# Kernel tuning notes

Measured on AMD Instinct MI355X. Metric: run time of the kernel, lower is better.

The kernel has to match this reference:

```python
import jax, jax.numpy as jnp
import numpy as np

N = 100000            # total buses
H = 64                # hidden_channels
OUT = 4               # out_channels
E = 100000            # edges per relation
EPF = 800000          # power-flow edges
# node-type global index ranges: SB, PV, PQ, NB
TYPE_RANGES = [(0, 10000), (10000, 30000), (30000, 70000), (70000, 100000)]
# 14 unique relations (src_type, dst_type) matching the HeteroConv dict order
RELS = [(0,1),(0,2),(0,3),(1,2),(1,3),(2,3),(1,0),(2,0),(3,0),(2,1),(3,2),(1,1),(2,2),(3,3)]
NUM_REL = len(RELS)


def custom_sigmoid(v, lo, hi, slope=0.1):
    mid = (lo + hi) * 0.5
    s = 1.0 / (1.0 + jnp.exp(-slope * (v - mid)))
    return (s - 0.5) * (hi - lo) + mid


def setup_inputs() -> dict:
    key = jax.random.key(0)
    ks = jax.random.split(key, 32)
    # node features (kept away from 0: x[:,0] is a divisor in the PF update)
    x = jax.random.uniform(ks[0], (N, 4)) + 0.5
    # constraints: [v_lo, v_hi, s_max, p_lo, p_hi, q_lo, q_hi] with lo < hi
    b = jax.random.uniform(ks[1], (N, 7))
    constraints = jnp.stack([b[:, 0], b[:, 0] + 1.0, b[:, 2],
                             b[:, 3] - 1.0, b[:, 3] + 1.0,
                             b[:, 5] - 1.0, b[:, 5] + 1.0], axis=1)
    rng = np.random.default_rng(0)
    edge_src = np.stack([rng.integers(TYPE_RANGES[s][0], TYPE_RANGES[s][1], size=E)
                         for s, _ in RELS]).astype(np.int32)
    edge_dst = np.stack([rng.integers(TYPE_RANGES[d][0], TYPE_RANGES[d][1], size=E)
                         for _, d in RELS]).astype(np.int32)
    edge_attr = jax.random.uniform(ks[2], (NUM_REL, E, 2)) + 0.5   # (R, X) > 0
    pf_i = jnp.asarray(rng.integers(0, N, size=EPF).astype(np.int32))
    pf_j = jnp.asarray(rng.integers(0, N, size=EPF).astype(np.int32))
    pf_attr = jax.random.uniform(ks[3], (EPF, 2)) + 0.5

    def W(k, *shape):
        return jax.random.normal(k, shape) * 0.05

    p = {}
    # layer 0 convs: in=4 ; layer 1 convs: in=H. Per-relation stacked weights.
    names = ['Wq', 'bq', 'Wk', 'bk', 'Wv', 'bv', 'We', 'Ws', 'bs']
    for layer, din in [(0, 4), (1, H)]:
        kk = jax.random.split(ks[4 + layer], 9)
        shapes = [(NUM_REL, din, H), (NUM_REL, H), (NUM_REL, din, H), (NUM_REL, H),
                  (NUM_REL, din, H), (NUM_REL, H), (NUM_REL, 2, H),
                  (NUM_REL, din, H), (NUM_REL, H)]
        for nm, sk, sh in zip(names, kk, shapes):
            p[f'{nm}{layer}'] = W(sk, *sh)
    Wlin = W(ks[6], H, OUT)
    return dict(x=x, constraints=constraints,
                edge_src=jnp.asarray(edge_src), edge_dst=jnp.asarray(edge_dst),
                edge_attr=edge_attr, pf_i=pf_i, pf_j=pf_j, pf_attr=pf_attr,
                Wlin=Wlin, **p)


def _hetero_layer(h, params, edge_src, edge_dst, edge_attr):
    """One HeteroConv(TransformerConv, aggr='sum') layer over global node array h[N,din]."""
    Wq, bq, Wk, bk, Wv, bv, We, Ws, bs = params
    n = h.shape[0]
    scale = Wq.shape[-1] ** -0.5
    out = jnp.zeros((n, Wq.shape[-1]), h.dtype)
    for r in range(NUM_REL):
        dlo, dhi = TYPE_RANGES[RELS[r][1]]
        s, d = edge_src[r], edge_dst[r]
        hs = h[s]                                    # [E, din] gathered src feats
        eemb = edge_attr[r] @ We[r]                  # lin_edge (no bias)
        kmat = hs @ Wk[r] + bk[r] + eemb             # key_j + edge
        vmat = hs @ Wv[r] + bv[r]                    # value_j
        q_dst = h[dlo:dhi] @ Wq[r] + bq[r]           # query on dst-type nodes only
        alpha = jnp.sum(q_dst[d - dlo] * kmat, axis=-1) * scale
        # segment softmax over incoming edges per dst node (per relation)
        m = jax.ops.segment_max(alpha, d, num_segments=n)
        a = jnp.exp(alpha - m[d])
        den = jax.ops.segment_sum(a, d, num_segments=n)
        a = a / (den[d] + 1e-16)
        out = out + jax.ops.segment_sum(a[:, None] * (vmat + eemb), d, num_segments=n)
        # root/skip connection (per relation, summed by HeteroConv aggr='sum')
        out = out.at[dlo:dhi].add(h[dlo:dhi] @ Ws[r] + bs[r])
    return out


def _forward(x, constraints, edge_attr, pf_attr, p0, p1, Wlin,
             edge_src, edge_dst, pf_i, pf_j):
    h = jax.nn.relu(_hetero_layer(x, p0, edge_src, edge_dst, edge_attr))
    h = jax.nn.relu(_hetero_layer(h, p1, edge_src, edge_dst, edge_attr))
    out = h @ Wlin                                   # [N, 4], lin (no bias)
    # vectorized per-bus power flow (edge-parallel gather-compute-scatter)
    V = jnp.abs(out[:, 0])
    th = out[:, 1]
    r_, x_ = pf_attr[:, 0], pf_attr[:, 1]
    den = r_ * r_ + x_ * x_
    G = r_ / den
    B = -x_ / den
    dlt = th[pf_j] - th[pf_i]
    cd, sd = jnp.cos(dlt), jnp.sin(dlt)
    vv = V[pf_i] * V[pf_j]
    P = jax.ops.segment_sum(vv * (G * cd + B * sd), pf_i, num_segments=N)
    Q = jax.ops.segment_sum(vv * (G * sd - B * cd), pf_i, num_segments=N)
    o0 = custom_sigmoid(V, constraints[:, 0], constraints[:, 1]) / x[:, 0]
    o2 = custom_sigmoid(P, constraints[:, 3], constraints[:, 4])
    o3 = custom_sigmoid(Q, constraints[:, 5], constraints[:, 6])
    return out.at[:, 0].set(o0).at[:, 2].set(o2).at[:, 3].set(o3)


def reference(x, constraints, edge_src, edge_dst, edge_attr, pf_i, pf_j, pf_attr,
              Wq0, bq0, Wk0, bk0, Wv0, bv0, We0, Ws0, bs0,
              Wq1, bq1, Wk1, bk1, Wv1, bv1, We1, Ws1, bs1, Wlin):
    p0 = (Wq0, bq0, Wk0, bk0, Wv0, bv0, We0, Ws0, bs0)
    p1 = (Wq1, bq1, Wk1, bk1, Wv1, bv1, We1, Ws1, bs1)
    return _forward(x, constraints, edge_attr, pf_attr, p0, p1, Wlin,
                    edge_src, edge_dst, pf_i, pf_j)
```

## Files before the change

### kernel.cpp

```cpp
#include <hip/hip_runtime.h>
#include <hip/hip_bf16.h>

#define NREL 14
#define NE     100000
#define NEDGE  (NREL*NE)
#define NN     100000
#define EPF    800000
#define NQ     370000
#define NB1    ((NQ + 1023) / 1024)
#define QWAVES 5786
#define TWAVES 1564

__device__ __constant__ int d_dlo[NREL]   = {10000,30000,70000,30000,70000,70000,0,0,0,10000,30000,10000,30000,70000};
__device__ __constant__ int d_qoff[NREL+1]= {0,20000,60000,90000,130000,160000,190000,200000,210000,220000,240000,280000,300000,340000,370000};
__device__ __constant__ int d_qwoff[NREL+1]={0,313,938,1407,2032,2501,2970,3127,3284,3441,3754,4379,4692,5317,5786};
__device__ __constant__ int d_trel[4][4]  = {{6,7,8,-1},{0,9,11,-1},{1,3,10,12},{2,4,5,13}};
__device__ __constant__ int d_ntrel[4]    = {3,3,4,4};
__device__ __constant__ int d_tbase[5]    = {0,10000,30000,70000,100000};
__device__ __constant__ int d_twoff[5]    = {0,157,470,1095,1564};

__device__ __forceinline__ float csig(float v, float lo, float hi) {
    float mid = 0.5f * (lo + hi);
    float s = 1.0f / (1.0f + expf(-0.1f * (v - mid)));
    return (s - 0.5f) * (hi - lo) + mid;
}

template<int K>
__device__ __forceinline__ void stage_in(
    float* sIn, const float* __restrict__ src, int l0, int n, int tid)
{
    if (K == 4) {
        if (tid < 64) {
            int lcl = min(l0 + tid, n - 1);
            float4 v = *(const float4*)(src + (long)lcl * 4);
            sIn[0 * 64 + tid] = v.x; sIn[1 * 64 + tid] = v.y;
            sIn[2 * 64 + tid] = v.z; sIn[3 * 64 + tid] = v.w;
        }
    } else {
        int row = tid >> 2, q = tid & 3;
        int lcl = min(l0 + row, n - 1);
        const float* p = src + (long)lcl * 64 + q * 16;
        #pragma unroll
        for (int kk = 0; kk < 4; ++kk) {
            float4 v = *(const float4*)(p + kk * 4);
            int k = q * 16 + kk * 4;
            sIn[(k + 0) * 64 + row] = v.x;
            sIn[(k + 1) * 64 + row] = v.y;
            sIn[(k + 2) * 64 + row] = v.z;
            sIn[(k + 3) * 64 + row] = v.w;
        }
    }
}

template<int K>
__device__ __forceinline__ void stage_w(
    float* sW, const float* __restrict__ src, int tid)
{
    for (int i = tid * 4; i < K * 64; i += 1024)
        *(float4*)(sW + i) = *(const float4*)(src + i);
}

template<int K>
__device__ __forceinline__ void mma_t(
    float acc[4][4], const float* sIn, const float* sW, int r0, int c0)
{
    for (int k = 0; k < K; ++k) {
        float4 a = *(const float4*)(sIn + k * 64 + r0);
        float4 b = *(const float4*)(sW + k * 64 + c0);
        acc[0][0] = fmaf(a.x, b.x, acc[0][0]);
        acc[0][1] = fmaf(a.x, b.y, acc[0][1]);
        acc[0][2] = fmaf(a.x, b.z, acc[0][2]);
        acc[0][3] = fmaf(a.x, b.w, acc[0][3]);
        acc[1][0] = fmaf(a.y, b.x, acc[1][0]);
        acc[1][1] = fmaf(a.y, b.y, acc[1][1]);
        acc[1][2] = fmaf(a.y, b.z, acc[1][2]);
        acc[1][3] = fmaf(a.y, b.w, acc[1][3]);
        acc[2][0] = fmaf(a.z, b.x, acc[2][0]);
        acc[2][1] = fmaf(a.z, b.y, acc[2][1]);
        acc[2][2] = fmaf(a.z, b.z, acc[2][2]);
        acc[2][3] = fmaf(a.z, b.w, acc[2][3]);
        acc[3][0] = fmaf(a.w, b.x, acc[3][0]);
        acc[3][1] = fmaf(a.w, b.y, acc[3][1]);
        acc[3][2] = fmaf(a.w, b.z, acc[3][2]);
        acc[3][3] = fmaf(a.w, b.w, acc[3][3]);
    }
}

template<int DIN>
__global__ __launch_bounds__(256) void combine_skip(
    const float* __restrict__ Ws, float* __restrict__ Wc)
{
    int tid = blockIdx.x * blockDim.x + threadIdx.x;
    if (tid >= 4 * DIN * 64) return;
    int t = tid / (DIN * 64), o = tid % (DIN * 64);
    float s = 0.f;
    for (int ri = 0; ri < d_ntrel[t]; ++ri) s += Ws[d_trel[t][ri] * DIN * 64 + o];
    Wc[tid] = s;
}

template<int DIN>
__global__ __launch_bounds__(256) void mk_m2t(
    const float* __restrict__ Wk, const float* __restrict__ Wq,
    float* __restrict__ M2T)
{
    int tid = blockIdx.x * blockDim.x + threadIdx.x;
    if (tid >= NREL * DIN * DIN) return;
    int r = tid / (DIN * DIN), rem = tid % (DIN * DIN);
    int i = rem / DIN, j = rem % DIN;
    const float* wki = Wk + (long)r * DIN * 64 + i * 64;
    const float* wqj = Wq + (long)r * DIN * 64 + j * 64;
    float s = 0.f;
    for (int c = 0; c < 64; ++c) s = fmaf(wki[c], wqj[c], s);
    M2T[(long)r * DIN * DIN + j * DIN + i] = s;
}

template<int DIN>
__global__ __launch_bounds__(256) void mk_vecs(
    const float* __restrict__ Wk, const float* __restrict__ Wq,
    const float* __restrict__ bq, const float* __restrict__ bk,
    const float* __restrict__ We, float* __restrict__ vec4)
{
    int tid = blockIdx.x * blockDim.x + threadIdx.x;
    if (tid >= NREL * 4 * DIN) return;
    int r = tid / (4 * DIN), rem = tid % (4 * DIN);
    int k = rem / DIN, i = rem % DIN;
    const float* row; const float* v;
    if (k == 0) { row = Wk + (long)r * DIN * 64 + i * 64; v = bq + r * 64; }
    else {
        row = Wq + (long)r * DIN * 64 + i * 64;
        v = (k == 1) ? We + r * 128 : (k == 2) ? We + r * 128 + 64 : bk + r * 64;
    }
    float s = 0.f;
    for (int c = 0; c < 64; ++c) s = fmaf(row[c], v[c], s);
    vec4[tid] = s;
}

__global__ __launch_bounds__(64) void mk_scl(
    const float* __restrict__ bq, const float* __restrict__ bk,
    const float* __restrict__ We, float* __restrict__ scl)
{
    int r = blockIdx.x * blockDim.x + threadIdx.x;
    if (r >= NREL) return;
    float s0 = 0.f, s1 = 0.f, sb = 0.f;
    for (int c = 0; c < 64; ++c) {
        float b = bq[r * 64 + c];
        s0 = fmaf(b, We[r * 128 + c], s0);
        s1 = fmaf(b, We[r * 128 + 64 + c], s1);
        sb = fmaf(b, bk[r * 64 + c], sb);
    }
    scl[4 * r] = s0; scl[4 * r + 1] = s1; scl[4 * r + 2] = sb; scl[4 * r + 3] = 0.f;
}

__global__ __launch_bounds__(256) void dstprep4(
    const float* __restrict__ h, const float* __restrict__ M2T,
    const float* __restrict__ vec4, const float* __restrict__ scl,
    float* __restrict__ ug, float* __restrict__ scal)
{
    int idx = blockIdx.x * blockDim.x + threadIdx.x;
    if (idx >= NQ) return;
    int r = 0;
    while (r < NREL - 1 && idx >= d_qoff[r + 1]) ++r;
    int node = d_dlo[r] + (idx - d_qoff[r]);
    float4 hv = ((const float4*)h)[node];
    const float* m2 = M2T + (long)r * 16;
    const float* vb = vec4 + (long)r * 16;
    float u[4];
    #pragma unroll
    for (int c = 0; c < 4; ++c)
        u[c] = vb[c] + hv.x * m2[c] + hv.y * m2[4 + c] + hv.z * m2[8 + c] + hv.w * m2[12 + c];
    float sc0 = scl[4*r]   + hv.x*vb[4]  + hv.y*vb[5]  + hv.z*vb[6]  + hv.w*vb[7];
    float sc1 = scl[4*r+1] + hv.x*vb[8]  + hv.y*vb[9]  + hv.z*vb[10] + hv.w*vb[11];
    float scb = scl[4*r+2] + hv.x*vb[12] + hv.y*vb[13] + hv.z*vb[14] + hv.w*vb[15];
    ((float4*)ug)[idx] = make_float4(u[0], u[1], u[2], u[3]);
    ((float4*)scal)[idx] = make_float4(sc0, sc1, scb, 0.f);
}

__global__ __launch_bounds__(256) void dstprep_g(
    const float* __restrict__ h, const float* __restrict__ M2T,
    const float* __restrict__ vec4, const float* __restrict__ scl,
    float* __restrict__ ug, float* __restrict__ scal)
{
    __shared__ float sIn[64 * 64];
    __shared__ float sW[64 * 64];
    int blk = blockIdx.x, tid = threadIdx.x;
    int r = 0;
    while (r < NREL - 1 && blk >= d_qwoff[r + 1]) ++r;
    int l0 = (blk - d_qwoff[r]) * 64;
    int nd = d_qoff[r + 1] - d_qoff[r];
    stage_in<64>(sIn, h + (long)d_dlo[r] * 64, l0, nd, tid);
    stage_w<64>(sW, M2T + (long)r * 4096, tid);
    __syncthreads();
    int tx = tid & 15, ty = tid >> 4;
    int r0 = ty * 4, c0 = tx * 4;
    float4 bias = *(const float4*)(vec4 + (long)r * 256 + c0);
    float acc[4][4];
    #pragma unroll
    for (int i = 0; i < 4; ++i) {
        acc[i][0] = bias.x; acc[i][1] = bias.y; acc[i][2] = bias.z; acc[i][3] = bias.w;
    }
    mma_t<64>(acc, sIn, sW, r0, c0);
    #pragma unroll
    for (int i = 0; i < 4; ++i) {
        int lr = l0 + r0 + i;
        if (lr < nd)
            *(float4*)(ug + (long)(d_qoff[r] + lr) * 64 + c0) =
                make_float4(acc[i][0], acc[i][1], acc[i][2], acc[i][3]);
    }
    if (tid < 64) {
        const float* w1p = vec4 + (long)r * 256 + 64;
        const float* w2p = vec4 + (long)r * 256 + 128;
        const float* w3p = vec4 + (long)r * 256 + 192;
        float s0 = 0.f, s1 = 0.f, s2 = 0.f;
        for (int k = 0; k < 64; ++k) {
            float hv = sIn[k * 64 + tid];
            s0 = fmaf(hv, w1p[k], s0);
            s1 = fmaf(hv, w2p[k], s1);
            s2 = fmaf(hv, w3p[k], s2);
        }
        int lr = l0 + tid;
        if (lr < nd)
            ((float4*)scal)[d_qoff[r] + lr] =
                make_float4(s0 + scl[4*r], s1 + scl[4*r+1], s2 + scl[4*r+2], 0.f);
    }
}

__global__ __launch_bounds__(256) void csr_count(
    const int* __restrict__ edst, int* __restrict__ cur)
{
    int tid = blockIdx.x * blockDim.x + threadIdx.x;
    if (tid >= NEDGE) return;
    int r = tid / NE;
    atomicAdd(&cur[d_qoff[r] + edst[tid] - d_dlo[r]], 1);
}

__global__ __launch_bounds__(1024) void scan1(
    const int* __restrict__ cur, int* __restrict__ rowst, int* __restrict__ bsum)
{
    __shared__ int s[1024];
    int t = threadIdx.x, g = blockIdx.x * 1024 + t;
    s[t] = g < NQ ? cur[g] : 0;
    __syncthreads();
    for (int o = 1; o < 1024; o <<= 1) {
        int x = t >= o ? s[t - o] : 0;
        __syncthreads();
        s[t] += x;
        __syncthreads();
    }
    if (g < NQ) rowst[g + 1] = s[t];
    if (t == 1023) bsum[blockIdx.x] = s[1023];
}

__global__ __launch_bounds__(512) void scan2(int* __restrict__ bsum)
{
    __shared__ int s[512];
    int t = threadIdx.x;
    s[t] = t < NB1 ? bsum[t] : 0;
    __syncthreads();
    for (int o = 1; o < 512; o <<= 1) {
        int x = t >= o ? s[t - o] : 0;
        __syncthreads();
        s[t] += x;
        __syncthreads();
    }
    if (t < NB1) bsum[t] = (t == 0) ? 0 : s[t - 1];
}

__global__ __launch_bounds__(256) void scan3(
    const int* __restrict__ bsum, int* __restrict__ rowst)
{
    int g = blockIdx.x * blockDim.x + threadIdx.x;
    if (g == 0) rowst[0] = 0;
    if (g < NQ) rowst[g + 1] += bsum[g >> 10];
}

__global__ __launch_bounds__(256) void csr_fill(
    const int* __restrict__ edst, const int* __restrict__ rowst,
    int* __restrict__ cur, int* __restrict__ elist)
{
    int tid = blockIdx.x * blockDim.x + threadIdx.x;
    if (tid >= NEDGE) return;
    int r = tid / NE;
    int idx = d_qoff[r] + edst[tid] - d_dlo[r];
    int pos = rowst[idx] + atomicAdd(&cur[idx], 1);
    elist[pos] = tid;
}

__global__ __launch_bounds__(256) void gfuse_t4(
    const float* __restrict__ h, const float* __restrict__ scal,
    const int* __restrict__ esrc, const float* __restrict__ eattr,
    const int* __restrict__ rowst, const int* __restrict__ elist,
    float* __restrict__ ug, float* __restrict__ gm)
{
    int idx = blockIdx.x * blockDim.x + threadIdx.x;
    if (idx >= NQ) return;
    int e0 = rowst[idx], e1 = rowst[idx + 1];
    if (e0 == e1) {
        ((float4*)ug)[idx] = make_float4(0.f, 0.f, 0.f, 0.f);
        gm[2 * (long)idx] = 0.f; gm[2 * (long)idx + 1] = 0.f;
        return;
    }
    float4 u = ((const float4*)ug)[idx];
    float4 sc = ((const float4*)scal)[idx];
    float m = -3.4e38f, den = 0.f, m0 = 0.f, m1 = 0.f;
    float gx = 0.f, gy = 0.f, gz = 0.f, gw = 0.f;
    for (int e = e0; e < e1; ++e) {
        int eid = elist[e];
        float4 hs = ((const float4*)h)[esrc[eid]];
        float2 ea = *(const float2*)(eattr + 2 * (long)eid);
        float alpha = 0.125f * (hs.x*u.x + hs.y*u.y + hs.z*u.z + hs.w*u.w
                                + sc.z + ea.x * sc.x + ea.y * sc.y);
        float nm = fmaxf(m, alpha);
        float s = expf(m - nm);
        float a = expf(alpha - nm);
        m = nm;
        den = den * s + a;
        gx = gx * s + a * hs.x; gy = gy * s + a * hs.y;
        gz = gz * s + a * hs.z; gw = gw * s + a * hs.w;
        m0 = m0 * s + a * ea.x; m1 = m1 * s + a * ea.y;
    }
    float inv = 1.f / (den + 1e-16f);
    ((float4*)ug)[idx] = make_float4(gx*inv, gy*inv, gz*inv, gw*inv);
    gm[2 * (long)idx] = m0 * inv; gm[2 * (long)idx + 1] = m1 * inv;
}

__global__ __launch_bounds__(256) void gfuse_q(
    const float* __restrict__ h, const float* __restrict__ scal,
    const int* __restrict__ esrc, const float* __restrict__ eattr,
    const int* __restrict__ rowst, const int* __restrict__ elist,
    float* __restrict__ ug, float* __restrict__ gm)
{
    int idx = (blockIdx.x * blockDim.x + threadIdx.x) >> 4;
    int ql  = threadIdx.x & 15;
    if (idx >= NQ) return;
    int e0 = rowst[idx], e1 = rowst[idx + 1];
    long ubase = (long)idx * 64 + ql * 4;
    if (e0 == e1) {
        *(float4*)(ug + ubase) = make_float4(0.f, 0.f, 0.f, 0.f);
        if (ql == 0) { gm[2*(long)idx] = 0.f; gm[2*(long)idx+1] = 0.f; }
        return;
    }
    float4 u = *(const float4*)(ug + ubase);
    float4 sc = ((const float4*)scal)[idx];
    float m = -3.4e38f, den = 0.f, m0 = 0.f, m1 = 0.f;
    float4 g = make_float4(0.f, 0.f, 0.f, 0.f);
    for (int e = e0; e < e1; ++e) {
        int eid = elist[e];
        int s = esrc[eid];
        float2 ea = *(const float2*)(eattr + 2 * (long)eid);
        float4 hs = *(const float4*)(h + (long)s * 64 + ql * 4);
        float p = hs.x*u.x + hs.y*u.y + hs.z*u.z + hs.w*u.w;
        p += __shfl_xor(p, 1);
        p += __shfl_xor(p, 2);
        p += __shfl_xor(p, 4);
        p += __shfl_xor(p, 8);
        float alpha = 0.125f * (p + sc.z + ea.x * sc.x + ea.y * sc.y);
        float nm = fmaxf(m, alpha);
        float s0 = expf(m - nm);
        float a  = expf(alpha - nm);
        m = nm;
        den = den * s0 + a;
        g.x = g.x * s0 + a * hs.x;
        g.y = g.y * s0 + a * hs.y;
        g.z = g.z * s0 + a * hs.z;
        g.w = g.w * s0 + a * hs.w;
        m0 = m0 * s0 + a * ea.x;
        m1 = m1 * s0 + a * ea.y;
    }
    float inv = 1.f / (den + 1e-16f);
    *(float4*)(ug + ubase) = make_float4(g.x*inv, g.y*inv, g.z*inv, g.w*inv);
    if (ql == 0) { gm[2*(long)idx] = m0 * inv; gm[2*(long)idx+1] = m1 * inv; }
}

template<int K, int RELU>
__global__ __launch_bounds__(256) void combine_g(
    const float* __restrict__ h, const float* __restrict__ Wc,
    const float* __restrict__ bs, const float* __restrict__ Wv,
    const float* __restrict__ bv, const float* __restrict__ We,
    const float* __restrict__ ug, const float* __restrict__ gm,
    const int* __restrict__ rowst, float* __restrict__ outp)
{
    __shared__ float sIn[K * 64];
    __shared__ float sW[K * 64];
    __shared__ float sHe[64], sG0[64], sG1[64];
    int blk = blockIdx.x, tid = threadIdx.x;
    int t = 0;
    while (t < 3 && blk >= d_twoff[t + 1]) ++t;
    int l0 = (blk - d_twoff[t]) * 64;
    int nt = d_tbase[t + 1] - d_tbase[t];
    int tx = tid & 15, ty = tid >> 4;
    int r0 = ty * 4, c0 = tx * 4;
    float acc[4][4];
    #pragma unroll
    for (int i = 0; i < 4; ++i) {
        acc[i][0] = 0.f; acc[i][1] = 0.f; acc[i][2] = 0.f; acc[i][3] = 0.f;
    }
    stage_in<K>(sIn, h + (long)d_tbase[t] * K, l0, nt, tid);
    stage_w<K>(sW, Wc + (long)t * K * 64, tid);
    __syncthreads();
    mma_t<K>(acc, sIn, sW, r0, c0);
    int nr = d_ntrel[t];
    for (int ri = 0; ri < nr; ++ri) {
        int rr = d_trel[t][ri];
        __syncthreads();
        stage_in<K>(sIn, ug + (long)d_qoff[rr] * K, l0, nt, tid);
        stage_w<K>(sW, Wv + (long)rr * K * 64, tid);
        if (tid < 64) {
            int lcl = min(l0 + tid, nt - 1);
            long idx = d_qoff[rr] + lcl;
            sHe[tid] = (rowst[idx + 1] > rowst[idx]) ? 1.f : 0.f;
            sG0[tid] = gm[2 * idx];
            sG1[tid] = gm[2 * idx + 1];
        }
        __syncthreads();
        mma_t<K>(acc, sIn, sW, r0, c0);
        float4 bsr = *(const float4*)(bs + rr * 64 + c0);
        float4 bvr = *(const float4*)(bv + rr * 64 + c0);
        float4 w0  = *(const float4*)(We + rr * 128 + c0);
        float4 w1  = *(const float4*)(We + rr * 128 + 64 + c0);
        #pragma unroll
        for (int i = 0; i < 4; ++i) {
            float he = sHe[r0 + i], g0 = sG0[r0 + i], g1 = sG1[r0 + i];
            acc[i][0] += bsr.x + he * bvr.x + g0 * w0.x + g1 * w1.x;
            acc[i][1] += bsr.y + he * bvr.y + g0 * w0.y + g1 * w1.y;
            acc[i][2] += bsr.z + he * bvr.z + g0 * w0.z + g1 * w1.z;
            acc[i][3] += bsr.w + he * bvr.w + g0 * w0.w + g1 * w1.w;
        }
    }
    #pragma unroll
    for (int i = 0; i < 4; ++i) {
        int lr = l0 + r0 + i;
        if (lr < nt) {
            float4 v = make_float4(acc[i][0], acc[i][1], acc[i][2], acc[i][3]);
            if (RELU) {
                v.x = fmaxf(v.x, 0.f); v.y = fmaxf(v.y, 0.f);
                v.z = fmaxf(v.z, 0.f); v.w = fmaxf(v.w, 0.f);
            }
            *(float4*)(outp + (long)(d_tbase[t] + lr) * 64 + c0) = v;
        }
    }
}

__global__ __launch_bounds__(256) void head(
    const float* __restrict__ acc, const float* __restrict__ Wlin,
    float* __restrict__ out4)
{
    int wid  = (blockIdx.x * blockDim.x + threadIdx.x) >> 6;
    int lane = threadIdx.x & 63;
    if (wid >= NN) return;
    float hv = fmaxf(acc[(long)wid * 64 + lane], 0.f);
    float4 w = ((const float4*)Wlin)[lane];
    float p0 = hv * w.x, p1 = hv * w.y, p2 = hv * w.z, p3 = hv * w.w;
    #pragma unroll
    for (int m = 32; m > 0; m >>= 1) {
        p0 += __shfl_xor(p0, m);
        p1 += __shfl_xor(p1, m);
        p2 += __shfl_xor(p2, m);
        p3 += __shfl_xor(p3, m);
    }
    if (lane == 0) {
        out4[4 * (long)wid + 0] = p0;
        out4[4 * (long)wid + 1] = p1;
        out4[4 * (long)wid + 2] = p2;
        out4[4 * (long)wid + 3] = p3;
    }
}

__global__ __launch_bounds__(256) void pf_accum(
    const int* __restrict__ pfi, const int* __restrict__ pfj,
    const float* __restrict__ pfa, const float* __restrict__ out4,
    float* __restrict__ Pb, float* __restrict__ Qp)
{
    int e = blockIdx.x * blockDim.x + threadIdx.x;
    if (e >= EPF) return;
    int i = pfi[e], j = pfj[e];
    float r = pfa[2 * (long)e], x = pfa[2 * (long)e + 1];
    float dn = r * r + x * x;
    float G = r / dn, B = -x / dn;
    float thi = out4[4 * (long)i + 1], thj = out4[4 * (long)j + 1];
    float Vi = fabsf(out4[4 * (long)i]), Vj = fabsf(out4[4 * (long)j]);
    float dlt = thj - thi;
    float cd = cosf(dlt), sd = sinf(dlt);
    float vv = Vi * Vj;
    atomicAdd(&Pb[i], vv * (G * cd + B * sd));
    atomicAdd(&Qp[i], vv * (G * sd - B * cd));
}

__global__ __launch_bounds__(256) void final_out(
    const float* __restrict__ out4, const float* __restrict__ cons,
    const float* __restrict__ xin, const float* __restrict__ Pb,
    const float* __restrict__ Qp, float* __restrict__ out)
{
    int n = blockIdx.x * blockDim.x + threadIdx.x;
    if (n >= NN) return;
    const float* c = cons + 7 * (long)n;
    float th = out4[4 * (long)n + 1];
    float V  = fabsf(out4[4 * (long)n + 0]);
    float o0 = csig(V, c[0], c[1]) / xin[4 * (long)n + 0];
    float o2 = csig(Pb[n], c[3], c[4]);
    float o3 = csig(Qp[n], c[5], c[6]);
    out[4 * (long)n + 0] = o0;
    out[4 * (long)n + 1] = th;
    out[4 * (long)n + 2] = o2;
    out[4 * (long)n + 3] = o3;
}

extern "C" void kernel_launch(void* const* d_in, const int* in_sizes, int n_in,
                              void* d_out, int out_size, void* d_ws, size_t ws_size,
                              hipStream_t stream) {
    const float* xin  = (const float*)d_in[0];
    const float* cons = (const float*)d_in[1];
    const int*   esrc = (const int*)d_in[2];
    const int*   edst = (const int*)d_in[3];
    const float* eatt = (const float*)d_in[4];
    const int*   pfi  = (const int*)d_in[5];
    const int*   pfj  = (const int*)d_in[6];
    const float* pfa  = (const float*)d_in[7];

    const float* Wlin;
    int wb;
    if (in_sizes[8] == 256) { Wlin = (const float*)d_in[8];  wb = 9; }
    else                    { Wlin = (const float*)d_in[26]; wb = 8; }
    const float* Wq0 = (const float*)d_in[wb + 0];
    const float* bq0 = (const float*)d_in[wb + 1];
    const float* Wk0 = (const float*)d_in[wb + 2];
    const float* bk0 = (const float*)d_in[wb + 3];
    const float* Wv0 = (const float*)d_in[wb + 4];
    const float* bv0 = (const float*)d_in[wb + 5];
    const float* We0 = (const float*)d_in[wb + 6];
    const float* Ws0 = (const float*)d_in[wb + 7];
    const float* bs0 = (const float*)d_in[wb + 8];
    const float* Wq1 = (const float*)d_in[wb + 9];
    const float* bq1 = (const float*)d_in[wb + 10];
    const float* Wk1 = (const float*)d_in[wb + 11];
    const float* bk1 = (const float*)d_in[wb + 12];
    const float* Wv1 = (const float*)d_in[wb + 13];
    const float* bv1 = (const float*)d_in[wb + 14];
    const float* We1 = (const float*)d_in[wb + 15];
    const float* Ws1 = (const float*)d_in[wb + 16];
    const float* bs1 = (const float*)d_in[wb + 17];

    float* w = (float*)d_ws;
    size_t off = 0;
    float* h1     = w + off; off += (size_t)NN * 64;
    float* acc    = w + off; off += (size_t)NN * 64;
    float* ug     = w + off; off += (size_t)NQ * 64;
    float* scal   = w + off; off += (size_t)NQ * 4;
    float* gm     = w + off; off += (size_t)NQ * 2;
    int*   rowst  = (int*)(w + off); off += NQ + 1;
    int*   cur    = (int*)(w + off); off += NQ;
    int*   bsum   = (int*)(w + off); off += 512;
    int*   elist  = (int*)(w + off); off += NEDGE;
    float* M2T    = w + off; off += (size_t)NREL * 64 * 64;
    float* vec4   = w + off; off += (size_t)NREL * 4 * 64;
    float* sclr   = w + off; off += NREL * 4;
    float* Wc0    = w + off; off += 4 * 4 * 64;
    float* Wc1    = w + off; off += 4 * 64 * 64;
    float* Pb     = w + off; off += NN;
    float* Qp     = w + off; off += NN;
    float* out4   = w + off; off += (size_t)NN * 4;
    if (ws_size < off * sizeof(float)) return;

    const int nodeWaveBlks = (NN + 3) / 4;
    const int gqBlocks = ((size_t)NQ * 16 + 255) / 256;

    hipMemsetAsync(cur, 0, (size_t)NQ * 4, stream);
    hipMemsetAsync(Pb,  0, (size_t)NN * 4, stream);
    hipMemsetAsync(Qp,  0, (size_t)NN * 4, stream);

    combine_skip<4> <<<(4*4*64 + 255)/256, 256, 0, stream>>>(Ws0, Wc0);
    combine_skip<64><<<(4*64*64 + 255)/256, 256, 0, stream>>>(Ws1, Wc1);

    csr_count<<<(NEDGE + 255)/256, 256, 0, stream>>>(edst, cur);
    scan1<<<NB1, 1024, 0, stream>>>(cur, rowst, bsum);
    scan2<<<1, 512, 0, stream>>>(bsum);
    scan3<<<(NQ + 255)/256, 256, 0, stream>>>(bsum, rowst);
    hipMemsetAsync(cur, 0, (size_t)NQ * 4, stream);
    csr_fill<<<(NEDGE + 255)/256, 256, 0, stream>>>(edst, rowst, cur, elist);

    mk_m2t<4><<<(NREL*16 + 255)/256, 256, 0, stream>>>(Wk0, Wq0, M2T);
    mk_vecs<4><<<(NREL*16 + 255)/256, 256, 0, stream>>>(Wk0, Wq0, bq0, bk0, We0, vec4);
    mk_scl<<<1, 64, 0, stream>>>(bq0, bk0, We0, sclr);
    dstprep4<<<(NQ + 255)/256, 256, 0, stream>>>(xin, M2T, vec4, sclr, ug, scal);
    gfuse_t4<<<(NQ + 255)/256, 256, 0, stream>>>(xin, scal, esrc, eatt, rowst, elist, ug, gm);
    combine_g<4,1><<<TWAVES, 256, 0, stream>>>(xin, Wc0, bs0, Wv0, bv0, We0, ug, gm, rowst, h1);

    mk_m2t<64><<<(NREL*64*64 + 255)/256, 256, 0, stream>>>(Wk1, Wq1, M2T);
    mk_vecs<64><<<(NREL*4*64 + 255)/256, 256, 0, stream>>>(Wk1, Wq1, bq1, bk1, We1, vec4);
    mk_scl<<<1, 64, 0, stream>>>(bq1, bk1, We1, sclr);
    dstprep_g<<<QWAVES, 256, 0, stream>>>(h1, M2T, vec4, sclr, ug, scal);
    gfuse_q<<<gqBlocks, 256, 0, stream>>>(h1, scal, esrc, eatt, rowst, elist, ug, gm);
    combine_g<64,0><<<TWAVES, 256, 0, stream>>>(h1, Wc1, bs1, Wv1, bv1, We1, ug, gm, rowst, acc);

    head<<<nodeWaveBlks, 256, 0, stream>>>(acc, Wlin, out4);
    pf_accum<<<(EPF + 255)/256, 256, 0, stream>>>(pfi, pfj, pfa, out4, Pb, Qp);
    final_out<<<(NN + 255)/256, 256, 0, stream>>>(out4, cons, xin, Pb, Qp, (float*)d_out);
}
```

Baseline: 722.2 us.

## Fuse destination-side query projection into attention gather kernels for both layers

Folds the per-destination projection (dstprep4 and dstprep_g) into the edge-softmax gather kernels, so the projected query vector and its scalar terms stay in registers or shared memory instead of round-tripping through global ug/scal buffers. For layer 1, each 256-thread block computes the 64x64 tile projection into shared memory and then runs the 16-lane-per-destination online softmax over 64 destinations in four groups. This removes two kernel launches and about 100 MB of global traffic. In exchange, each block has a longer serial tail, load balance across variable-degree destinations gets worse, and the 32 KB shared-memory footprint may lower occupancy during the gather phase.

```diff
diff --git a/kernel.cpp b/kernel.cpp
--- a/kernel.cpp
+++ b/kernel.cpp
@@ -151,79 +151,6 @@
     scl[4 * r] = s0; scl[4 * r + 1] = s1; scl[4 * r + 2] = sb; scl[4 * r + 3] = 0.f;
 }
 
-__global__ __launch_bounds__(256) void dstprep4(
-    const float* __restrict__ h, const float* __restrict__ M2T,
-    const float* __restrict__ vec4, const float* __restrict__ scl,
-    float* __restrict__ ug, float* __restrict__ scal)
-{
-    int idx = blockIdx.x * blockDim.x + threadIdx.x;
-    if (idx >= NQ) return;
-    int r = 0;
-    while (r < NREL - 1 && idx >= d_qoff[r + 1]) ++r;
-    int node = d_dlo[r] + (idx - d_qoff[r]);
-    float4 hv = ((const float4*)h)[node];
-    const float* m2 = M2T + (long)r * 16;
-    const float* vb = vec4 + (long)r * 16;
-    float u[4];
-    #pragma unroll
-    for (int c = 0; c < 4; ++c)
-        u[c] = vb[c] + hv.x * m2[c] + hv.y * m2[4 + c] + hv.z * m2[8 + c] + hv.w * m2[12 + c];
-    float sc0 = scl[4*r]   + hv.x*vb[4]  + hv.y*vb[5]  + hv.z*vb[6]  + hv.w*vb[7];
-    float sc1 = scl[4*r+1] + hv.x*vb[8]  + hv.y*vb[9]  + hv.z*vb[10] + hv.w*vb[11];
-    float scb = scl[4*r+2] + hv.x*vb[12] + hv.y*vb[13] + hv.z*vb[14] + hv.w*vb[15];
-    ((float4*)ug)[idx] = make_float4(u[0], u[1], u[2], u[3]);
-    ((float4*)scal)[idx] = make_float4(sc0, sc1, scb, 0.f);
-}
-
-__global__ __launch_bounds__(256) void dstprep_g(
-    const float* __restrict__ h, const float* __restrict__ M2T,
-    const float* __restrict__ vec4, const float* __restrict__ scl,
-    float* __restrict__ ug, float* __restrict__ scal)
-{
-    __shared__ float sIn[64 * 64];
-    __shared__ float sW[64 * 64];
-    int blk = blockIdx.x, tid = threadIdx.x;
-    int r = 0;
-    while (r < NREL - 1 && blk >= d_qwoff[r + 1]) ++r;
-    int l0 = (blk - d_qwoff[r]) * 64;
-    int nd = d_qoff[r + 1] - d_qoff[r];
-    stage_in<64>(sIn, h + (long)d_dlo[r] * 64, l0, nd, tid);
-    stage_w<64>(sW, M2T + (long)r * 4096, tid);
-    __syncthreads();
-    int tx = tid & 15, ty = tid >> 4;
-    int r0 = ty * 4, c0 = tx * 4;
-    float4 bias = *(const float4*)(vec4 + (long)r * 256 + c0);
-    float acc[4][4];
-    #pragma unroll
-    for (int i = 0; i < 4; ++i) {
-        acc[i][0] = bias.x; acc[i][1] = bias.y; acc[i][2] = bias.z; acc[i][3] = bias.w;
-    }
-    mma_t<64>(acc, sIn, sW, r0, c0);
-    #pragma unroll
-    for (int i = 0; i < 4; ++i) {
-        int lr = l0 + r0 + i;
-        if (lr < nd)
-            *(float4*)(ug + (long)(d_qoff[r] + lr) * 64 + c0) =
-                make_float4(acc[i][0], acc[i][1], acc[i][2], acc[i][3]);
-    }
-    if (tid < 64) {
-        const float* w1p = vec4 + (long)r * 256 + 64;
-        const float* w2p = vec4 + (long)r * 256 + 128;
-        const float* w3p = vec4 + (long)r * 256 + 192;
-        float s0 = 0.f, s1 = 0.f, s2 = 0.f;
-        for (int k = 0; k < 64; ++k) {
-            float hv = sIn[k * 64 + tid];
-            s0 = fmaf(hv, w1p[k], s0);
-            s1 = fmaf(hv, w2p[k], s1);
-            s2 = fmaf(hv, w3p[k], s2);
-        }
-        int lr = l0 + tid;
-        if (lr < nd)
-            ((float4*)scal)[d_qoff[r] + lr] =
-                make_float4(s0 + scl[4*r], s1 + scl[4*r+1], s2 + scl[4*r+2], 0.f);
-    }
-}
-
 __global__ __launch_bounds__(256) void csr_count(
     const int* __restrict__ edst, int* __restrict__ cur)
 {
@@ -285,8 +212,9 @@
     elist[pos] = tid;
 }
 
-__global__ __launch_bounds__(256) void gfuse_t4(
-    const float* __restrict__ h, const float* __restrict__ scal,
+__global__ __launch_bounds__(256) void gfuse_t40(
+    const float* __restrict__ h, const float* __restrict__ M2T,
+    const float* __restrict__ vec4, const float* __restrict__ scl,
     const int* __restrict__ esrc, const float* __restrict__ eattr,
     const int* __restrict__ rowst, const int* __restrict__ elist,
     float* __restrict__ ug, float* __restrict__ gm)
@@ -299,8 +227,20 @@
         gm[2 * (long)idx] = 0.f; gm[2 * (long)idx + 1] = 0.f;
         return;
     }
-    float4 u = ((const float4*)ug)[idx];
-    float4 sc = ((const float4*)scal)[idx];
+    int r = 0;
+    while (r < NREL - 1 && idx >= d_qoff[r + 1]) ++r;
+    int node = d_dlo[r] + (idx - d_qoff[r]);
+    float4 hv = ((const float4*)h)[node];
+    const float* m2 = M2T + (long)r * 16;
+    const float* vb = vec4 + (long)r * 16;
+    float4 u;
+    u.x = vb[0] + hv.x*m2[0]  + hv.y*m2[4]  + hv.z*m2[8]  + hv.w*m2[12];
+    u.y = vb[1] + hv.x*m2[1]  + hv.y*m2[5]  + hv.z*m2[9]  + hv.w*m2[13];
+    u.z = vb[2] + hv.x*m2[2]  + hv.y*m2[6]  + hv.z*m2[10] + hv.w*m2[14];
+    u.w = vb[3] + hv.x*m2[3]  + hv.y*m2[7]  + hv.z*m2[11] + hv.w*m2[15];
+    float sc0 = scl[4*r]   + hv.x*vb[4]  + hv.y*vb[5]  + hv.z*vb[6]  + hv.w*vb[7];
+    float sc1 = scl[4*r+1] + hv.x*vb[8]  + hv.y*vb[9]  + hv.z*vb[10] + hv.w*vb[11];
+    float scb = scl[4*r+2] + hv.x*vb[12] + hv.y*vb[13] + hv.z*vb[14] + hv.w*vb[15];
     float m = -3.4e38f, den = 0.f, m0 = 0.f, m1 = 0.f;
     float gx = 0.f, gy = 0.f, gz = 0.f, gw = 0.f;
     for (int e = e0; e < e1; ++e) {
@@ -308,7 +248,7 @@
         float4 hs = ((const float4*)h)[esrc[eid]];
         float2 ea = *(const float2*)(eattr + 2 * (long)eid);
         float alpha = 0.125f * (hs.x*u.x + hs.y*u.y + hs.z*u.z + hs.w*u.w
-                                + sc.z + ea.x * sc.x + ea.y * sc.y);
+                                + scb + ea.x * sc0 + ea.y * sc1);
         float nm = fmaxf(m, alpha);
         float s = expf(m - nm);
         float a = expf(alpha - nm);
@@ -323,52 +263,100 @@
     gm[2 * (long)idx] = m0 * inv; gm[2 * (long)idx + 1] = m1 * inv;
 }
 
-__global__ __launch_bounds__(256) void gfuse_q(
-    const float* __restrict__ h, const float* __restrict__ scal,
+__global__ __launch_bounds__(256) void gfuse_g(
+    const float* __restrict__ h, const float* __restrict__ M2T,
+    const float* __restrict__ vec4, const float* __restrict__ scl,
     const int* __restrict__ esrc, const float* __restrict__ eattr,
     const int* __restrict__ rowst, const int* __restrict__ elist,
     float* __restrict__ ug, float* __restrict__ gm)
 {
-    int idx = (blockIdx.x * blockDim.x + threadIdx.x) >> 4;
-    int ql  = threadIdx.x & 15;
-    if (idx >= NQ) return;
-    int e0 = rowst[idx], e1 = rowst[idx + 1];
-    long ubase = (long)idx * 64 + ql * 4;
-    if (e0 == e1) {
-        *(float4*)(ug + ubase) = make_float4(0.f, 0.f, 0.f, 0.f);
-        if (ql == 0) { gm[2*(long)idx] = 0.f; gm[2*(long)idx+1] = 0.f; }
-        return;
-    }
-    float4 u = *(const float4*)(ug + ubase);
-    float4 sc = ((const float4*)scal)[idx];
-    float m = -3.4e38f, den = 0.f, m0 = 0.f, m1 = 0.f;
-    float4 g = make_float4(0.f, 0.f, 0.f, 0.f);
-    for (int e = e0; e < e1; ++e) {
-        int eid = elist[e];
-        int s = esrc[eid];
-        float2 ea = *(const float2*)(eattr + 2 * (long)eid);
-        float4 hs = *(const float4*)(h + (long)s * 64 + ql * 4);
-        float p = hs.x*u.x + hs.y*u.y + hs.z*u.z + hs.w*u.w;
-        p += __shfl_xor(p, 1);
-        p += __shfl_xor(p, 2);
-        p += __shfl_xor(p, 4);
-        p += __shfl_xor(p, 8);
-        float alpha = 0.125f * (p + sc.z + ea.x * sc.x + ea.y * sc.y);
-        float nm = fmaxf(m, alpha);
-        float s0 = expf(m - nm);
-        float a  = expf(alpha - nm);
-        m = nm;
-        den = den * s0 + a;
-        g.x = g.x * s0 + a * hs.x;
-        g.y = g.y * s0 + a * hs.y;
-        g.z = g.z * s0 + a * hs.z;
-        g.w = g.w * s0 + a * hs.w;
-        m0 = m0 * s0 + a * ea.x;
-        m1 = m1 * s0 + a * ea.y;
-    }
-    float inv = 1.f / (den + 1e-16f);
-    *(float4*)(ug + ubase) = make_float4(g.x*inv, g.y*inv, g.z*inv, g.w*inv);
-    if (ql == 0) { gm[2*(long)idx] = m0 * inv; gm[2*(long)idx+1] = m1 * inv; }
+    __shared__ float sA[64 * 64];
+    __shared__ float sB[64 * 64];
+    __shared__ float sS[64 * 4];
+    int blk = blockIdx.x, tid = threadIdx.x;
+    int r = 0;
+    while (r < NREL - 1 && blk >= d_qwoff[r + 1]) ++r;
+    int l0 = (blk - d_qwoff[r]) * 64;
+    int nd = d_qoff[r + 1] - d_qoff[r];
+
+    stage_in<64>(sA, h + (long)d_dlo[r] * 64, l0, nd, tid);
+    stage_w<64>(sB, M2T + (long)r * 4096, tid);
+    __syncthreads();
+    int tx = tid & 15, ty = tid >> 4;
+    int r0 = ty * 4, c0 = tx * 4;
+    float4 bias = *(const float4*)(vec4 + (long)r * 256 + c0);
+    float acc[4][4];
+    #pragma unroll
+    for (int i = 0; i < 4; ++i) {
+        acc[i][0] = bias.x; acc[i][1] = bias.y; acc[i][2] = bias.z; acc[i][3] = bias.w;
+    }
+    mma_t<64>(acc, sA, sB, r0, c0);
+    __syncthreads();
+    if (tid < 64) {
+        const float* w1p = vec4 + (long)r * 256 + 64;
+        const float* w2p = vec4 + (long)r * 256 + 128;
+        const float* w3p = vec4 + (long)r * 256 + 192;
+        float s0 = 0.f, s1 = 0.f, s2 = 0.f;
+        for (int k = 0; k < 64; ++k) {
+            float hv = sA[k * 64 + tid];
+            s0 = fmaf(hv, w1p[k], s0);
+            s1 = fmaf(hv, w2p[k], s1);
+            s2 = fmaf(hv, w3p[k], s2);
+        }
+        *(float4*)(sS + tid * 4) =
+            make_float4(s0 + scl[4*r], s1 + scl[4*r+1], s2 + scl[4*r+2], 0.f);
+    }
+    __syncthreads();
+    #pragma unroll
+    for (int i = 0; i < 4; ++i)
+        *(float4*)(sA + (r0 + i) * 64 + c0) =
+            make_float4(acc[i][0], acc[i][1], acc[i][2], acc[i][3]);
+    __syncthreads();
+
+    int ql = tid & 15;
+    for (int grp = 0; grp < 4; ++grp) {
+        int dl = grp * 16 + (tid >> 4);
+        int lcl = l0 + dl;
+        if (lcl >= nd) continue;
+        long idx = d_qoff[r] + lcl;
+        int e0 = rowst[idx], e1 = rowst[idx + 1];
+        long ubase = (long)idx * 64 + ql * 4;
+        if (e0 == e1) {
+            *(float4*)(ug + ubase) = make_float4(0.f, 0.f, 0.f, 0.f);
+            if (ql == 0) { gm[2*idx] = 0.f; gm[2*idx+1] = 0.f; }
+            continue;
+        }
+        float4 u = *(const float4*)(sA + dl * 64 + ql * 4);
+        float4 sc = *(const float4*)(sS + dl * 4);
+        float m = -3.4e38f, den = 0.f, m0 = 0.f, m1 = 0.f;
+        float4 g = make_float4(0.f, 0.f, 0.f, 0.f);
+        for (int e = e0; e < e1; ++e) {
+            int eid = elist[e];
+            int s = esrc[eid];
+            float2 ea = *(const float2*)(eattr + 2 * (long)eid);
+            float4 hs = *(const float4*)(h + (long)s * 64 + ql * 4);
+            float p = hs.x*u.x + hs.y*u.y + hs.z*u.z + hs.w*u.w;
+            p += __shfl_xor(p, 1);
+            p += __shfl_xor(p, 2);
+            p += __shfl_xor(p, 4);
+            p += __shfl_xor(p, 8);
+            float alpha = 0.125f * (p + sc.z + ea.x * sc.x + ea.y * sc.y);
+            float nm = fmaxf(m, alpha);
+            float s0 = expf(m - nm);
+            float a  = expf(alpha - nm);
+            m = nm;
+            den = den * s0 + a;
+            g.x = g.x * s0 + a * hs.x;
+            g.y = g.y * s0 + a * hs.y;
+            g.z = g.z * s0 + a * hs.z;
+            g.w = g.w * s0 + a * hs.w;
+            m0 = m0 * s0 + a * ea.x;
+            m1 = m1 * s0 + a * ea.y;
+        }
+        float inv = 1.f / (den + 1e-16f);
+        *(float4*)(ug + ubase) = make_float4(g.x*inv, g.y*inv, g.z*inv, g.w*inv);
+        if (ql == 0) { gm[2*idx] = m0 * inv; gm[2*idx+1] = m1 * inv; }
+    }
 }
 
 template<int K, int RELU>
@@ -544,7 +532,6 @@
     float* h1     = w + off; off += (size_t)NN * 64;
     float* acc    = w + off; off += (size_t)NN * 64;
     float* ug     = w + off; off += (size_t)NQ * 64;
-    float* scal   = w + off; off += (size_t)NQ * 4;
     float* gm     = w + off; off += (size_t)NQ * 2;
     int*   rowst  = (int*)(w + off); off += NQ + 1;
     int*   cur    = (int*)(w + off); off += NQ;
@@ -561,7 +548,6 @@
     if (ws_size < off * sizeof(float)) return;
 
     const int nodeWaveBlks = (NN + 3) / 4;
-    const int gqBlocks = ((size_t)NQ * 16 + 255) / 256;
 
     hipMemsetAsync(cur, 0, (size_t)NQ * 4, stream);
     hipMemsetAsync(Pb,  0, (size_t)NN * 4, stream);
@@ -580,15 +566,13 @@
     mk_m2t<4><<<(NREL*16 + 255)/256, 256, 0, stream>>>(Wk0, Wq0, M2T);
     mk_vecs<4><<<(NREL*16 + 255)/256, 256, 0, stream>>>(Wk0, Wq0, bq0, bk0, We0, vec4);
     mk_scl<<<1, 64, 0, stream>>>(bq0, bk0, We0, sclr);
-    dstprep4<<<(NQ + 255)/256, 256, 0, stream>>>(xin, M2T, vec4, sclr, ug, scal);
-    gfuse_t4<<<(NQ + 255)/256, 256, 0, stream>>>(xin, scal, esrc, eatt, rowst, elist, ug, gm);
+    gfuse_t40<<<(NQ + 255)/256, 256, 0, stream>>>(xin, M2T, vec4, sclr, esrc, eatt, rowst, elist, ug, gm);
     combine_g<4,1><<<TWAVES, 256, 0, stream>>>(xin, Wc0, bs0, Wv0, bv0, We0, ug, gm, rowst, h1);
 
     mk_m2t<64><<<(NREL*64*64 + 255)/256, 256, 0, stream>>>(Wk1, Wq1, M2T);
     mk_vecs<64><<<(NREL*4*64 + 255)/256, 256, 0, stream>>>(Wk1, Wq1, bq1, bk1, We1, vec4);
     mk_scl<<<1, 64, 0, stream>>>(bq1, bk1, We1, sclr);
-    dstprep_g<<<QWAVES, 256, 0, stream>>>(h1, M2T, vec4, sclr, ug, scal);
-    gfuse_q<<<gqBlocks, 256, 0, stream>>>(h1, scal, esrc, eatt, rowst, elist, ug, gm);
+    gfuse_g<<<QWAVES, 256, 0, stream>>>(h1, M2T, vec4, sclr, esrc, eatt, rowst, elist, ug, gm);
     combine_g<64,0><<<TWAVES, 256, 0, stream>>>(h1, Wc1, bs1, Wv1, bv1, We1, ug, gm, rowst, acc);
 
     head<<<nodeWaveBlks, 256, 0, stream>>>(acc, Wlin, out4);
```

After: 784.8 us. +8.7%, slower.
